# Kernel optimization log

Measured on AMD Instinct MI355X. Metric: run time of the kernel, lower is better.

The kernel has to match this reference:

```python
import jax, jax.numpy as jnp
import numpy as np

B, T, D, H, A = 1, 262144, 8, 64, 4  # batch, seq_len, state_dim, hidden, n_actions


def setup_inputs() -> dict:
    key = jax.random.key(0)
    ks = jax.random.split(key, 10)
    s = lambda k, shape, sc: jax.random.normal(k, shape, dtype=jnp.float32) * sc
    return {
        "x": jax.random.normal(ks[0], (B, T, D), dtype=jnp.float32),
        # encoder MLP (Dense->tanh, Dense->tanh)
        "W1": s(ks[1], (D, H), 0.5), "b1": jnp.zeros((H,), jnp.float32),
        "W2": s(ks[2], (H, H), 0.15), "b2": jnp.zeros((H,), jnp.float32),
        # SimpleRNN params: h_t = tanh(x_t @ Wx + h_{t-1} @ Wh + b_rnn)
        "Wx": s(ks[3], (H, H), 0.15), "Wh": s(ks[4], (H, H), 0.1),
        "b_rnn": jnp.zeros((H,), jnp.float32),
        # means head
        "Wm": s(ks[5], (H, A), 0.01), "bm": jnp.zeros((A,), jnp.float32),
    }


def reference(x, W1, b1, W2, b2, Wx, Wh, b_rnn, Wm, bm):
    # Masking(mask_value=0): a timestep is masked if ALL features == 0
    mask = jnp.any(x != 0.0, axis=-1)  # [B, T] bool
    # TimeDistributed encoder (applies pointwise over time -> plain batched matmul)
    h1 = jnp.tanh(x @ W1 + b1)          # [B, T, H]
    h2 = jnp.tanh(h1 @ W2 + b2)         # [B, T, H]
    # Precompute input contribution to the RNN outside the scan (efficient form)
    xz = h2 @ Wx + b_rnn                # [B, T, H]

    def step(h, inp):
        z, m = inp                       # z: [B, H], m: [B]
        h_new = jnp.tanh(z + h @ Wh)
        # masked timesteps: carry previous state through (Keras RNN masking semantics)
        h = jnp.where(m[:, None], h_new, h)
        return h, h

    h0 = jnp.zeros((B, H), x.dtype)
    _, hs = jax.lax.scan(step, h0, (jnp.swapaxes(xz, 0, 1), jnp.swapaxes(mask, 0, 1)))
    hs = jnp.swapaxes(hs, 0, 1)          # [B, T, H]
    means = hs @ Wm + bm                 # [B, T, A]
    return means
```

## Files before the change

kernel.cpp:

```cpp
#include <hip/hip_runtime.h>
#include <hip/hip_bf16.h>

constexpr int T_LEN  = 262144;
constexpr int H      = 64;
constexpr int S_LEN  = 8;
constexpr int WARM   = 24;
constexpr int CHUNKS = T_LEN / S_LEN;
constexpr int NWAVE  = CHUNKS / 16;

typedef __attribute__((ext_vector_type(8))) short short8;
typedef __attribute__((ext_vector_type(4))) float f32x4;

__device__ __forceinline__ float fast_tanh(float x) {
    float e = __expf(2.0f * x);
    return 1.0f - 2.0f * __builtin_amdgcn_rcpf(e + 1.0f);
}
__device__ __forceinline__ unsigned short f2bf(float v) {
    unsigned u = __builtin_bit_cast(unsigned, v);
    return (unsigned short)((u + 0x7fffu + ((u >> 16) & 1u)) >> 16);
}
__device__ __forceinline__ float bf2f(unsigned short b) {
    return __builtin_bit_cast(float, (unsigned)b << 16);
}
__device__ __forceinline__ unsigned pack2(float a, float b) {
    return (unsigned)f2bf(a) | ((unsigned)f2bf(b) << 16);
}

__global__ __launch_bounds__(256) void encoder_kernel(
    const float* __restrict__ x,
    const float* __restrict__ W1, const float* __restrict__ b1,
    const float* __restrict__ W2, const float* __restrict__ b2,
    const float* __restrict__ Wx, const float* __restrict__ b_rnn,
    unsigned short* __restrict__ z_s, float* __restrict__ m_s)
{
    __shared__ uint4  bf2_[8 * 64];
    __shared__ uint4  bf3_[8 * 64];
    __shared__ float  act[64 * 65];

    const int tid = threadIdx.x;
    const int t0  = blockIdx.x * 64;

    {
        const int n  = tid & 63;
        const int kg = tid >> 6;
        float v2[16], v3[16];
        #pragma unroll
        for (int kk = 0; kk < 16; ++kk) {
            v2[kk] = W2[(kg * 16 + kk) * 64 + n];
            v3[kk] = Wx[(kg * 16 + kk) * 64 + n];
        }
        const int kh = kg >> 1;
        const int tn = n >> 4;
        #pragma unroll
        for (int s = 0; s < 2; ++s) {
            const int q    = (2 * kg + s) & 3;
            const int lane = q * 16 + (n & 15);
            uint4 o2, o3;
            o2.x = pack2(v2[s*8+0], v2[s*8+1]); o2.y = pack2(v2[s*8+2], v2[s*8+3]);
            o2.z = pack2(v2[s*8+4], v2[s*8+5]); o2.w = pack2(v2[s*8+6], v2[s*8+7]);
            o3.x = pack2(v3[s*8+0], v3[s*8+1]); o3.y = pack2(v3[s*8+2], v3[s*8+3]);
            o3.z = pack2(v3[s*8+4], v3[s*8+5]); o3.w = pack2(v3[s*8+6], v3[s*8+7]);
            bf2_[(tn * 2 + kh) * 64 + lane] = o2;
            bf3_[(tn * 2 + kh) * 64 + lane] = o3;
        }
    }

    {
        const int t  = tid & 63;
        const int jg = __builtin_amdgcn_readfirstlane(tid >> 6);
        const int j0 = jg * 16;
        const float4 xa = *(const float4*)(x + (size_t)(t0 + t) * 8);
        const float4 xb = *(const float4*)(x + (size_t)(t0 + t) * 8 + 4);
        const float xv[8] = {xa.x, xa.y, xa.z, xa.w, xb.x, xb.y, xb.z, xb.w};
        if (jg == 0) {
            bool nz = false;
            #pragma unroll
            for (int d = 0; d < 8; ++d) nz = nz || (xv[d] != 0.0f);
            m_s[t0 + t] = nz ? 1.0f : 0.0f;
        }
        float a1[16];
        #pragma unroll
        for (int jj = 0; jj < 16; ++jj) a1[jj] = b1[j0 + jj];
        #pragma unroll
        for (int d = 0; d < 8; ++d) {
            #pragma unroll
            for (int jj = 0; jj < 16; ++jj)
                a1[jj] = fmaf(xv[d], W1[d * 64 + j0 + jj], a1[jj]);
        }
        #pragma unroll
        for (int jj = 0; jj < 16; ++jj)
            act[t * 65 + j0 + jj] = fast_tanh(a1[jj]);
    }
    __syncthreads();

    const int l    = tid & 63;
    const int w    = tid >> 6;
    const int q    = l >> 4;
    const int l15  = l & 15;
    const int row0 = w * 16;

    {
        short8 af[2];
        #pragma unroll
        for (int kh = 0; kh < 2; ++kh) {
            short8 s;
            #pragma unroll
            for (int j = 0; j < 8; ++j)
                s[j] = (short)f2bf(act[(row0 + l15) * 65 + kh * 32 + q * 8 + j]);
            af[kh] = s;
        }
        f32x4 acc[4];
        #pragma unroll
        for (int tn = 0; tn < 4; ++tn) {
            f32x4 d = {0.f, 0.f, 0.f, 0.f};
            d = __builtin_amdgcn_mfma_f32_16x16x32_bf16(
                    af[0], __builtin_bit_cast(short8, bf2_[(tn * 2 + 0) * 64 + l]), d, 0, 0, 0);
            d = __builtin_amdgcn_mfma_f32_16x16x32_bf16(
                    af[1], __builtin_bit_cast(short8, bf2_[(tn * 2 + 1) * 64 + l]), d, 0, 0, 0);
            acc[tn] = d;
        }
        __builtin_amdgcn_wave_barrier();
        #pragma unroll
        for (int tn = 0; tn < 4; ++tn) {
            const float bb = b2[tn * 16 + l15];
            #pragma unroll
            for (int r = 0; r < 4; ++r)
                act[(row0 + q * 4 + r) * 65 + tn * 16 + l15] = fast_tanh(acc[tn][r] + bb);
        }
        __builtin_amdgcn_wave_barrier();
    }

    {
        short8 af[2];
        #pragma unroll
        for (int kh = 0; kh < 2; ++kh) {
            short8 s;
            #pragma unroll
            for (int j = 0; j < 8; ++j)
                s[j] = (short)f2bf(act[(row0 + l15) * 65 + kh * 32 + q * 8 + j]);
            af[kh] = s;
        }
        f32x4 acc[4];
        #pragma unroll
        for (int tn = 0; tn < 4; ++tn) {
            f32x4 d = {0.f, 0.f, 0.f, 0.f};
            d = __builtin_amdgcn_mfma_f32_16x16x32_bf16(
                    af[0], __builtin_bit_cast(short8, bf3_[(tn * 2 + 0) * 64 + l]), d, 0, 0, 0);
            d = __builtin_amdgcn_mfma_f32_16x16x32_bf16(
                    af[1], __builtin_bit_cast(short8, bf3_[(tn * 2 + 1) * 64 + l]), d, 0, 0, 0);
            acc[tn] = d;
        }
        __builtin_amdgcn_wave_barrier();
        #pragma unroll
        for (int tn = 0; tn < 4; ++tn) {
            const float bb = b_rnn[tn * 16 + l15];
            #pragma unroll
            for (int r = 0; r < 4; ++r)
                act[(row0 + q * 4 + r) * 65 + tn * 16 + l15] = acc[tn][r] + bb;
        }
    }
    __syncthreads();

    {
        const int ot = tid >> 2;
        const int og = (tid & 3) * 16;
        unsigned o[8];
        #pragma unroll
        for (int i = 0; i < 8; ++i)
            o[i] = pack2(act[ot * 65 + og + 2 * i], act[ot * 65 + og + 2 * i + 1]);
        uint4* dst = (uint4*)(z_s + (size_t)(t0 + ot) * 64 + og);
        dst[0] = make_uint4(o[0], o[1], o[2], o[3]);
        dst[1] = make_uint4(o[4], o[5], o[6], o[7]);
    }
}

__global__ __launch_bounds__(256) void rnn_kernel(
    const unsigned short* __restrict__ z_s, const float* __restrict__ m_s,
    const float* __restrict__ Wh, const float* __restrict__ Wm,
    const float* __restrict__ bm, float* __restrict__ out)
{
    __shared__ float pre[4][16 * 65];

    const int tid = threadIdx.x;
    const int w   = tid >> 6;
    const int l   = tid & 63;
    const int q   = l >> 4;
    const int l15 = l & 15;
    const int rw  = blockIdx.x * 4 + w;
    const int c   = rw * 16 + l15;

    short8 bfrag[8];
    #pragma unroll
    for (int tn = 0; tn < 4; ++tn) {
        #pragma unroll
        for (int kh = 0; kh < 2; ++kh) {
            short8 s;
            #pragma unroll
            for (int j = 0; j < 8; ++j)
                s[j] = (short)f2bf(Wh[(kh * 32 + q * 8 + j) * 64 + tn * 16 + l15]);
            bfrag[tn * 2 + kh] = s;
        }
    }
    short8 wmf[2];
    #pragma unroll
    for (int kh = 0; kh < 2; ++kh) {
        short8 s;
        #pragma unroll
        for (int j = 0; j < 8; ++j)
            s[j] = (l15 < 4) ? (short)f2bf(Wm[(kh * 32 + q * 8 + j) * 4 + l15]) : (short)0;
        wmf[kh] = s;
    }
    const float bm_l = (l15 < 4) ? bm[l15] : 0.0f;

    short8 hfrag[2];
    hfrag[0] = (short8)0;
    hfrag[1] = (short8)0;
    float* mypre = pre[w];

    auto t_of = [&](int st) -> size_t {
        long tt = (long)c * S_LEN + st;
        if (tt < 0) tt = 0;
        if (tt >= T_LEN) tt = T_LEN - 1;
        return (size_t)tt;
    };

    size_t tc = t_of(-WARM);
    uint4 zc0 = *(const uint4*)(z_s + tc * 64 + q * 8);
    uint4 zc1 = *(const uint4*)(z_s + tc * 64 + 32 + q * 8);
    float mc  = m_s[tc];

    auto body = [&](int st, bool means_prev) {
        const size_t tn_ = t_of(st + 1);
        const uint4 zn0 = *(const uint4*)(z_s + tn_ * 64 + q * 8);
        const uint4 zn1 = *(const uint4*)(z_s + tn_ * 64 + 32 + q * 8);
        const float mn  = m_s[tn_];

        f32x4 acc[4];
        #pragma unroll
        for (int tn = 0; tn < 4; ++tn) {
            f32x4 d = {0.f, 0.f, 0.f, 0.f};
            d = __builtin_amdgcn_mfma_f32_16x16x32_bf16(hfrag[0], bfrag[tn * 2 + 0], d, 0, 0, 0);
            d = __builtin_amdgcn_mfma_f32_16x16x32_bf16(hfrag[1], bfrag[tn * 2 + 1], d, 0, 0, 0);
            acc[tn] = d;
        }
        if (means_prev) {
            f32x4 a2 = {0.f, 0.f, 0.f, 0.f};
            a2 = __builtin_amdgcn_mfma_f32_16x16x32_bf16(hfrag[0], wmf[0], a2, 0, 0, 0);
            a2 = __builtin_amdgcn_mfma_f32_16x16x32_bf16(hfrag[1], wmf[1], a2, 0, 0, 0);
            if (l15 < 4) {
                #pragma unroll
                for (int r = 0; r < 4; ++r) {
                    const int cm = rw * 16 + q * 4 + r;
                    const size_t tp = (size_t)cm * S_LEN + (st - 1);
                    out[tp * 4 + l15] = a2[r] + bm_l;
                }
            }
        }
        #pragma unroll
        for (int tn = 0; tn < 4; ++tn)
            #pragma unroll
            for (int r = 0; r < 4; ++r)
                mypre[(q * 4 + r) * 65 + tn * 16 + l15] = acc[tn][r];
        __builtin_amdgcn_wave_barrier();

        const uint4 zvv[2] = {zc0, zc1};
        #pragma unroll
        for (int kh = 0; kh < 2; ++kh) {
            const unsigned short* zp = (const unsigned short*)&zvv[kh];
            short8 ns;
            #pragma unroll
            for (int j = 0; j < 8; ++j) {
                const float p = mypre[l15 * 65 + kh * 32 + q * 8 + j];
                ns[j] = (short)f2bf(fast_tanh(p + bf2f(zp[j])));
            }
            hfrag[kh] = (mc != 0.0f) ? ns : hfrag[kh];
        }
        __builtin_amdgcn_wave_barrier();

        zc0 = zn0; zc1 = zn1; mc = mn;
    };

    for (int st = -WARM; st < 0; ++st) body(st, false);
    if (c == 0) { hfrag[0] = (short8)0; hfrag[1] = (short8)0; }
    for (int st = 0; st < S_LEN; ++st) body(st, st >= 1);

    {
        f32x4 a2 = {0.f, 0.f, 0.f, 0.f};
        a2 = __builtin_amdgcn_mfma_f32_16x16x32_bf16(hfrag[0], wmf[0], a2, 0, 0, 0);
        a2 = __builtin_amdgcn_mfma_f32_16x16x32_bf16(hfrag[1], wmf[1], a2, 0, 0, 0);
        if (l15 < 4) {
            #pragma unroll
            for (int r = 0; r < 4; ++r) {
                const int cm = rw * 16 + q * 4 + r;
                const size_t tp = (size_t)cm * S_LEN + (S_LEN - 1);
                out[tp * 4 + l15] = a2[r] + bm_l;
            }
        }
    }
}

extern "C" void kernel_launch(void* const* d_in, const int* in_sizes, int n_in,
                              void* d_out, int out_size, void* d_ws, size_t ws_size,
                              hipStream_t stream) {
    const float* x     = (const float*)d_in[0];
    const float* W1    = (const float*)d_in[1];
    const float* b1    = (const float*)d_in[2];
    const float* W2    = (const float*)d_in[3];
    const float* b2    = (const float*)d_in[4];
    const float* Wx    = (const float*)d_in[5];
    const float* Wh    = (const float*)d_in[6];
    const float* b_rnn = (const float*)d_in[7];
    const float* Wm    = (const float*)d_in[8];
    const float* bm    = (const float*)d_in[9];
    float* out = (float*)d_out;

    unsigned short* z_s = (unsigned short*)d_ws;
    float*          m_s = (float*)((char*)d_ws + (size_t)T_LEN * H * 2);

    encoder_kernel<<<T_LEN / 64, 256, 0, stream>>>(x, W1, b1, W2, b2, Wx, b_rnn, z_s, m_s);
    rnn_kernel<<<NWAVE / 4, 256, 0, stream>>>(z_s, m_s, Wh, Wm, bm, out);
}
```

Before: 139.2 us.

## Move first encoder layer to MFMA, store z in fp32, per-wave encoder loop

The first encoder layer (x@W1) now runs on MFMA instead of scalar FMAs. x is split into bf16 high and low parts across the K dimension, which keeps close to fp32 accuracy. Each encoder block now processes 256 timesteps in four per-wave iterations using a per-wave padded LDS tile (stride 68) with vectorized LDS reads. The z intermediate is stored in fp32 rather than bf16, which doubles workspace traffic between the kernels but removes one rounding step. The RNN kernel is updated to read fp32 z with wider loads and vectorized LDS access.

Result: slower. 144.6 us (+3.9%).

```diff
diff --git a/kernel.cpp b/kernel.cpp
--- a/kernel.cpp
+++ b/kernel.cpp
@@ -7,6 +7,7 @@
 constexpr int WARM   = 24;
 constexpr int CHUNKS = T_LEN / S_LEN;
 constexpr int NWAVE  = CHUNKS / 16;
+constexpr int PRE_STRIDE = 68;
 
 typedef __attribute__((ext_vector_type(8))) short short8;
 typedef __attribute__((ext_vector_type(4))) float f32x4;
@@ -31,18 +32,22 @@
     const float* __restrict__ W1, const float* __restrict__ b1,
     const float* __restrict__ W2, const float* __restrict__ b2,
     const float* __restrict__ Wx, const float* __restrict__ b_rnn,
-    unsigned short* __restrict__ z_s, float* __restrict__ m_s)
+    float* __restrict__ z_s, float* __restrict__ m_s)
 {
-    __shared__ uint4  bf2_[8 * 64];
-    __shared__ uint4  bf3_[8 * 64];
-    __shared__ float  act[64 * 65];
+    __shared__ uint4 w1f[4 * 64];
+    __shared__ uint4 w2f[8 * 64];
+    __shared__ uint4 w3f[8 * 64];
+    __shared__ float pre_[4][16 * PRE_STRIDE];
 
     const int tid = threadIdx.x;
-    const int t0  = blockIdx.x * 64;
+    const int w   = tid >> 6;
+    const int l   = tid & 63;
+    const int q   = l >> 4;
+    const int l15 = l & 15;
 
     {
-        const int n  = tid & 63;
-        const int kg = tid >> 6;
+        const int n  = l;
+        const int kg = w;
         float v2[16], v3[16];
         #pragma unroll
         for (int kk = 0; kk < 16; ++kk) {
@@ -53,133 +58,169 @@
         const int tn = n >> 4;
         #pragma unroll
         for (int s = 0; s < 2; ++s) {
-            const int q    = (2 * kg + s) & 3;
-            const int lane = q * 16 + (n & 15);
+            const int qq   = (2 * kg + s) & 3;
+            const int lane = qq * 16 + (n & 15);
             uint4 o2, o3;
             o2.x = pack2(v2[s*8+0], v2[s*8+1]); o2.y = pack2(v2[s*8+2], v2[s*8+3]);
             o2.z = pack2(v2[s*8+4], v2[s*8+5]); o2.w = pack2(v2[s*8+6], v2[s*8+7]);
             o3.x = pack2(v3[s*8+0], v3[s*8+1]); o3.y = pack2(v3[s*8+2], v3[s*8+3]);
             o3.z = pack2(v3[s*8+4], v3[s*8+5]); o3.w = pack2(v3[s*8+6], v3[s*8+7]);
-            bf2_[(tn * 2 + kh) * 64 + lane] = o2;
-            bf3_[(tn * 2 + kh) * 64 + lane] = o3;
-        }
-    }
-
-    {
-        const int t  = tid & 63;
-        const int jg = __builtin_amdgcn_readfirstlane(tid >> 6);
-        const int j0 = jg * 16;
-        const float4 xa = *(const float4*)(x + (size_t)(t0 + t) * 8);
-        const float4 xb = *(const float4*)(x + (size_t)(t0 + t) * 8 + 4);
-        const float xv[8] = {xa.x, xa.y, xa.z, xa.w, xb.x, xb.y, xb.z, xb.w};
-        if (jg == 0) {
-            bool nz = false;
-            #pragma unroll
-            for (int d = 0; d < 8; ++d) nz = nz || (xv[d] != 0.0f);
-            m_s[t0 + t] = nz ? 1.0f : 0.0f;
-        }
-        float a1[16];
-        #pragma unroll
-        for (int jj = 0; jj < 16; ++jj) a1[jj] = b1[j0 + jj];
-        #pragma unroll
-        for (int d = 0; d < 8; ++d) {
-            #pragma unroll
-            for (int jj = 0; jj < 16; ++jj)
-                a1[jj] = fmaf(xv[d], W1[d * 64 + j0 + jj], a1[jj]);
-        }
-        #pragma unroll
-        for (int jj = 0; jj < 16; ++jj)
-            act[t * 65 + j0 + jj] = fast_tanh(a1[jj]);
+            w2f[(tn * 2 + kh) * 64 + lane] = o2;
+            w3f[(tn * 2 + kh) * 64 + lane] = o3;
+        }
+        uint4 o1 = make_uint4(0, 0, 0, 0);
+        if (q < 2) {
+            float v1[8];
+            #pragma unroll
+            for (int j = 0; j < 8; ++j) v1[j] = W1[j * 64 + w * 16 + l15];
+            o1.x = pack2(v1[0], v1[1]); o1.y = pack2(v1[2], v1[3]);
+            o1.z = pack2(v1[4], v1[5]); o1.w = pack2(v1[6], v1[7]);
+        }
+        w1f[w * 64 + l] = o1;
     }
     __syncthreads();
 
-    const int l    = tid & 63;
-    const int w    = tid >> 6;
-    const int q    = l >> 4;
-    const int l15  = l & 15;
-    const int row0 = w * 16;
-
-    {
+    float b1v[4], b2v[4], brv[4];
+    #pragma unroll
+    for (int tn = 0; tn < 4; ++tn) {
+        b1v[tn] = b1[tn * 16 + l15];
+        b2v[tn] = b2[tn * 16 + l15];
+        brv[tn] = b_rnn[tn * 16 + l15];
+    }
+
+    float* mypre = pre_[w];
+
+    #pragma unroll
+    for (int it = 0; it < 4; ++it) {
+        const int t0w = blockIdx.x * 256 + it * 64 + w * 16;
+
+        short8 a1 = (short8)0;
+        if (q < 2) {
+            const float4 xa = *(const float4*)(x + (size_t)(t0w + l15) * 8);
+            const float4 xb = *(const float4*)(x + (size_t)(t0w + l15) * 8 + 4);
+            const float xv[8] = {xa.x, xa.y, xa.z, xa.w, xb.x, xb.y, xb.z, xb.w};
+            if (q == 0) {
+                bool nz = false;
+                #pragma unroll
+                for (int d = 0; d < 8; ++d) nz = nz || (xv[d] != 0.0f);
+                m_s[t0w + l15] = nz ? 1.0f : 0.0f;
+                uint4 o;
+                o.x = pack2(xv[0], xv[1]); o.y = pack2(xv[2], xv[3]);
+                o.z = pack2(xv[4], xv[5]); o.w = pack2(xv[6], xv[7]);
+                a1 = __builtin_bit_cast(short8, o);
+            } else {
+                float lo[8];
+                #pragma unroll
+                for (int d = 0; d < 8; ++d) lo[d] = xv[d] - bf2f(f2bf(xv[d]));
+                uint4 o;
+                o.x = pack2(lo[0], lo[1]); o.y = pack2(lo[2], lo[3]);
+                o.z = pack2(lo[4], lo[5]); o.w = pack2(lo[6], lo[7]);
+                a1 = __builtin_bit_cast(short8, o);
+            }
+        }
+
+        {
+            f32x4 acc[4];
+            #pragma unroll
+            for (int tn = 0; tn < 4; ++tn)
+                acc[tn] = __builtin_amdgcn_mfma_f32_16x16x32_bf16(
+                    a1, __builtin_bit_cast(short8, w1f[tn * 64 + l]),
+                    (f32x4){0.f, 0.f, 0.f, 0.f}, 0, 0, 0);
+            #pragma unroll
+            for (int tn = 0; tn < 4; ++tn)
+                #pragma unroll
+                for (int r = 0; r < 4; ++r)
+                    mypre[(q * 4 + r) * PRE_STRIDE + tn * 16 + l15] =
+                        fast_tanh(acc[tn][r] + b1v[tn]);
+        }
+        __builtin_amdgcn_wave_barrier();
+
         short8 af[2];
         #pragma unroll
         for (int kh = 0; kh < 2; ++kh) {
-            short8 s;
-            #pragma unroll
-            for (int j = 0; j < 8; ++j)
-                s[j] = (short)f2bf(act[(row0 + l15) * 65 + kh * 32 + q * 8 + j]);
-            af[kh] = s;
-        }
-        f32x4 acc[4];
-        #pragma unroll
-        for (int tn = 0; tn < 4; ++tn) {
-            f32x4 d = {0.f, 0.f, 0.f, 0.f};
-            d = __builtin_amdgcn_mfma_f32_16x16x32_bf16(
-                    af[0], __builtin_bit_cast(short8, bf2_[(tn * 2 + 0) * 64 + l]), d, 0, 0, 0);
-            d = __builtin_amdgcn_mfma_f32_16x16x32_bf16(
-                    af[1], __builtin_bit_cast(short8, bf2_[(tn * 2 + 1) * 64 + l]), d, 0, 0, 0);
-            acc[tn] = d;
-        }
-        __builtin_amdgcn_wave_barrier();
-        #pragma unroll
-        for (int tn = 0; tn < 4; ++tn) {
-            const float bb = b2[tn * 16 + l15];
-            #pragma unroll
-            for (int r = 0; r < 4; ++r)
-                act[(row0 + q * 4 + r) * 65 + tn * 16 + l15] = fast_tanh(acc[tn][r] + bb);
-        }
-        __builtin_amdgcn_wave_barrier();
-    }
-
-    {
-        short8 af[2];
+            const uint4 r0 = *(const uint4*)(mypre + l15 * PRE_STRIDE + kh * 32 + q * 8);
+            const uint4 r1 = *(const uint4*)(mypre + l15 * PRE_STRIDE + kh * 32 + q * 8 + 4);
+            uint4 p;
+            p.x = pack2(__builtin_bit_cast(float, r0.x), __builtin_bit_cast(float, r0.y));
+            p.y = pack2(__builtin_bit_cast(float, r0.z), __builtin_bit_cast(float, r0.w));
+            p.z = pack2(__builtin_bit_cast(float, r1.x), __builtin_bit_cast(float, r1.y));
+            p.w = pack2(__builtin_bit_cast(float, r1.z), __builtin_bit_cast(float, r1.w));
+            af[kh] = __builtin_bit_cast(short8, p);
+        }
+        __builtin_amdgcn_wave_barrier();
+
+        {
+            f32x4 acc[4];
+            #pragma unroll
+            for (int tn = 0; tn < 4; ++tn) {
+                f32x4 d = {0.f, 0.f, 0.f, 0.f};
+                d = __builtin_amdgcn_mfma_f32_16x16x32_bf16(
+                        af[0], __builtin_bit_cast(short8, w2f[(tn * 2 + 0) * 64 + l]), d, 0, 0, 0);
+                d = __builtin_amdgcn_mfma_f32_16x16x32_bf16(
+                        af[1], __builtin_bit_cast(short8, w2f[(tn * 2 + 1) * 64 + l]), d, 0, 0, 0);
+                acc[tn] = d;
+            }
+            #pragma unroll
+            for (int tn = 0; tn < 4; ++tn)
+                #pragma unroll
+                for (int r = 0; r < 4; ++r)
+                    mypre[(q * 4 + r) * PRE_STRIDE + tn * 16 + l15] =
+                        fast_tanh(acc[tn][r] + b2v[tn]);
+        }
+        __builtin_amdgcn_wave_barrier();
+
         #pragma unroll
         for (int kh = 0; kh < 2; ++kh) {
-            short8 s;
-            #pragma unroll
-            for (int j = 0; j < 8; ++j)
-                s[j] = (short)f2bf(act[(row0 + l15) * 65 + kh * 32 + q * 8 + j]);
-            af[kh] = s;
-        }
-        f32x4 acc[4];
-        #pragma unroll
-        for (int tn = 0; tn < 4; ++tn) {
-            f32x4 d = {0.f, 0.f, 0.f, 0.f};
-            d = __builtin_amdgcn_mfma_f32_16x16x32_bf16(
-                    af[0], __builtin_bit_cast(short8, bf3_[(tn * 2 + 0) * 64 + l]), d, 0, 0, 0);
-            d = __builtin_amdgcn_mfma_f32_16x16x32_bf16(
-                    af[1], __builtin_bit_cast(short8, bf3_[(tn * 2 + 1) * 64 + l]), d, 0, 0, 0);
-            acc[tn] = d;
-        }
-        __builtin_amdgcn_wave_barrier();
-        #pragma unroll
-        for (int tn = 0; tn < 4; ++tn) {
-            const float bb = b_rnn[tn * 16 + l15];
-            #pragma unroll
-            for (int r = 0; r < 4; ++r)
-                act[(row0 + q * 4 + r) * 65 + tn * 16 + l15] = acc[tn][r] + bb;
-        }
-    }
-    __syncthreads();
-
-    {
-        const int ot = tid >> 2;
-        const int og = (tid & 3) * 16;
-        unsigned o[8];
-        #pragma unroll
-        for (int i = 0; i < 8; ++i)
-            o[i] = pack2(act[ot * 65 + og + 2 * i], act[ot * 65 + og + 2 * i + 1]);
-        uint4* dst = (uint4*)(z_s + (size_t)(t0 + ot) * 64 + og);
-        dst[0] = make_uint4(o[0], o[1], o[2], o[3]);
-        dst[1] = make_uint4(o[4], o[5], o[6], o[7]);
+            const uint4 r0 = *(const uint4*)(mypre + l15 * PRE_STRIDE + kh * 32 + q * 8);
+            const uint4 r1 = *(const uint4*)(mypre + l15 * PRE_STRIDE + kh * 32 + q * 8 + 4);
+            uint4 p;
+            p.x = pack2(__builtin_bit_cast(float, r0.x), __builtin_bit_cast(float, r0.y));
+            p.y = pack2(__builtin_bit_cast(float, r0.z), __builtin_bit_cast(float, r0.w));
+            p.z = pack2(__builtin_bit_cast(float, r1.x), __builtin_bit_cast(float, r1.y));
+            p.w = pack2(__builtin_bit_cast(float, r1.z), __builtin_bit_cast(float, r1.w));
+            af[kh] = __builtin_bit_cast(short8, p);
+        }
+        __builtin_amdgcn_wave_barrier();
+
+        {
+            f32x4 acc[4];
+            #pragma unroll
+            for (int tn = 0; tn < 4; ++tn) {
+                f32x4 d = {0.f, 0.f, 0.f, 0.f};
+                d = __builtin_amdgcn_mfma_f32_16x16x32_bf16(
+                        af[0], __builtin_bit_cast(short8, w3f[(tn * 2 + 0) * 64 + l]), d, 0, 0, 0);
+                d = __builtin_amdgcn_mfma_f32_16x16x32_bf16(
+                        af[1], __builtin_bit_cast(short8, w3f[(tn * 2 + 1) * 64 + l]), d, 0, 0, 0);
+                acc[tn] = d;
+            }
+            #pragma unroll
+            for (int tn = 0; tn < 4; ++tn)
+                #pragma unroll
+                for (int r = 0; r < 4; ++r)
+                    mypre[(q * 4 + r) * PRE_STRIDE + tn * 16 + l15] = acc[tn][r] + brv[tn];
+        }
+        __builtin_amdgcn_wave_barrier();
+
+        {
+            const int ot = l >> 2;
+            const int fq = l & 3;
+            const float* src = mypre + ot * PRE_STRIDE + fq * 16;
+            float* dst = z_s + (size_t)(t0w + ot) * 64 + fq * 16;
+            ((uint4*)dst)[0] = *(const uint4*)(src + 0);
+            ((uint4*)dst)[1] = *(const uint4*)(src + 4);
+            ((uint4*)dst)[2] = *(const uint4*)(src + 8);
+            ((uint4*)dst)[3] = *(const uint4*)(src + 12);
+        }
+        __builtin_amdgcn_wave_barrier();
     }
 }
 
 __global__ __launch_bounds__(256) void rnn_kernel(
-    const unsigned short* __restrict__ z_s, const float* __restrict__ m_s,
+    const float* __restrict__ z_s, const float* __restrict__ m_s,
     const float* __restrict__ Wh, const float* __restrict__ Wm,
     const float* __restrict__ bm, float* __restrict__ out)
 {
-    __shared__ float pre[4][16 * 65];
+    __shared__ float pre_[4][16 * PRE_STRIDE];
 
     const int tid = threadIdx.x;
     const int w   = tid >> 6;
@@ -215,7 +256,7 @@
     short8 hfrag[2];
     hfrag[0] = (short8)0;
     hfrag[1] = (short8)0;
-    float* mypre = pre[w];
+    float* mypre = pre_[w];
 
     auto t_of = [&](int st) -> size_t {
         long tt = (long)c * S_LEN + st;
@@ -224,16 +265,25 @@
         return (size_t)tt;
     };
 
-    size_t tc = t_of(-WARM);
-    uint4 zc0 = *(const uint4*)(z_s + tc * 64 + q * 8);
-    uint4 zc1 = *(const uint4*)(z_s + tc * 64 + 32 + q * 8);
-    float mc  = m_s[tc];
+    uint4 zc[4];
+    float mc;
+    {
+        const size_t tc = t_of(-WARM);
+        zc[0] = *(const uint4*)(z_s + tc * 64 + q * 8);
+        zc[1] = *(const uint4*)(z_s + tc * 64 + q * 8 + 4);
+        zc[2] = *(const uint4*)(z_s + tc * 64 + 32 + q * 8);
+        zc[3] = *(const uint4*)(z_s + tc * 64 + 32 + q * 8 + 4);
+        mc    = m_s[tc];
+    }
 
     auto body = [&](int st, bool means_prev) {
         const size_t tn_ = t_of(st + 1);
-        const uint4 zn0 = *(const uint4*)(z_s + tn_ * 64 + q * 8);
-        const uint4 zn1 = *(const uint4*)(z_s + tn_ * 64 + 32 + q * 8);
-        const float mn  = m_s[tn_];
+        uint4 zn[4];
+        zn[0] = *(const uint4*)(z_s + tn_ * 64 + q * 8);
+        zn[1] = *(const uint4*)(z_s + tn_ * 64 + q * 8 + 4);
+        zn[2] = *(const uint4*)(z_s + tn_ * 64 + 32 + q * 8);
+        zn[3] = *(const uint4*)(z_s + tn_ * 64 + 32 + q * 8 + 4);
+        const float mn = m_s[tn_];
 
         f32x4 acc[4];
         #pragma unroll
@@ -260,28 +310,35 @@
         for (int tn = 0; tn < 4; ++tn)
             #pragma unroll
             for (int r = 0; r < 4; ++r)
-                mypre[(q * 4 + r) * 65 + tn * 16 + l15] = acc[tn][r];
-        __builtin_amdgcn_wave_barrier();
-
-        const uint4 zvv[2] = {zc0, zc1};
+                mypre[(q * 4 + r) * PRE_STRIDE + tn * 16 + l15] = acc[tn][r];
+        __builtin_amdgcn_wave_barrier();
+
         #pragma unroll
         for (int kh = 0; kh < 2; ++kh) {
-            const unsigned short* zp = (const unsigned short*)&zvv[kh];
-            short8 ns;
-            #pragma unroll
-            for (int j = 0; j < 8; ++j) {
-                const float p = mypre[l15 * 65 + kh * 32 + q * 8 + j];
-                ns[j] = (short)f2bf(fast_tanh(p + bf2f(zp[j])));
-            }
+            const uint4 zlo = zc[kh * 2 + 0];
+            const uint4 zhi = zc[kh * 2 + 1];
+            const unsigned zd[8] = {zlo.x, zlo.y, zlo.z, zlo.w, zhi.x, zhi.y, zhi.z, zhi.w};
+            const uint4 r0 = *(const uint4*)(mypre + l15 * PRE_STRIDE + kh * 32 + q * 8);
+            const uint4 r1 = *(const uint4*)(mypre + l15 * PRE_STRIDE + kh * 32 + q * 8 + 4);
+            const unsigned pd[8] = {r0.x, r0.y, r0.z, r0.w, r1.x, r1.y, r1.z, r1.w};
+            float th[8];
+            #pragma unroll
+            for (int j = 0; j < 8; ++j)
+                th[j] = fast_tanh(__builtin_bit_cast(float, pd[j]) +
+                                  __builtin_bit_cast(float, zd[j]));
+            uint4 p;
+            p.x = pack2(th[0], th[1]); p.y = pack2(th[2], th[3]);
+            p.z = pack2(th[4], th[5]); p.w = pack2(th[6], th[7]);
+            const short8 ns = __builtin_bit_cast(short8, p);
             hfrag[kh] = (mc != 0.0f) ? ns : hfrag[kh];
         }
         __builtin_amdgcn_wave_barrier();
 
-        zc0 = zn0; zc1 = zn1; mc = mn;
+        zc[0] = zn[0]; zc[1] = zn[1]; zc[2] = zn[2]; zc[3] = zn[3]; mc = mn;
     };
 
     for (int st = -WARM; st < 0; ++st) body(st, false);
-    if (c == 0) { hfrag[0] = (short8)0; hfrag[1] = (short8)0; }
+    if (rw == 0 && l15 == 0) { hfrag[0] = (short8)0; hfrag[1] = (short8)0; }
     for (int st = 0; st < S_LEN; ++st) body(st, st >= 1);
 
     {
@@ -314,9 +371,9 @@
     const float* bm    = (const float*)d_in[9];
     float* out = (float*)d_out;
 
-    unsigned short* z_s = (unsigned short*)d_ws;
-    float*          m_s = (float*)((char*)d_ws + (size_t)T_LEN * H * 2);
-
-    encoder_kernel<<<T_LEN / 64, 256, 0, stream>>>(x, W1, b1, W2, b2, Wx, b_rnn, z_s, m_s);
+    float* z_s = (float*)d_ws;
+    float* m_s = (float*)((char*)d_ws + (size_t)T_LEN * H * 4);
+
+    encoder_kernel<<<T_LEN / 256, 256, 0, stream>>>(x, W1, b1, W2, b2, Wx, b_rnn, z_s, m_s);
     rnn_kernel<<<NWAVE / 4, 256, 0, stream>>>(z_s, m_s, Wh, Wm, bm, out);
 }
```
